# Performance work log

Hardware: AMD Instinct MI355X
Metric: run time of the kernel (lower is better)

## Reference

```python
import jax, jax.numpy as jnp
import numpy as np
from jax import lax

HEADS = 8
C, H, W = 64, 16, 16
D_K = C // HEADS
SCALE = 1.0 / np.sqrt(D_K * H * W).astype(np.float32)


def conv2d(x, w, b):
    # x: [N, C, H, W], w: [O, I, 3, 3], padding=1
    y = lax.conv_general_dilated(x, w, window_strides=(1, 1),
                                 padding=((1, 1), (1, 1)),
                                 dimension_numbers=('NCHW', 'OIHW', 'NCHW'))
    return y + b[None, :, None, None]


def _project(x, w, b, bs, seq):
    # x: [bs, seq, C, H, W] -> conv per frame -> [bs, heads, seq, d_k*H*W]
    y = conv2d(x.reshape(bs * seq, C, H, W), w, b)
    y = y.reshape(bs, seq, HEADS, D_K, H, W)
    y = jnp.transpose(y, (0, 2, 1, 3, 4, 5)).reshape(bs, HEADS, seq, D_K * H * W)
    return y


def setup_inputs() -> dict:
    key = jax.random.key(0)
    ks = jax.random.split(key, 11)
    shp = (2, 256, C, H, W)
    wstd = 1.0 / np.sqrt(C * 9)  # torch Conv2d default init scale
    inp = {
        'q': jax.random.normal(ks[0], shp, jnp.float32),
        'k': jax.random.normal(ks[1], shp, jnp.float32),
        'v': jax.random.normal(ks[2], shp, jnp.float32),
        'Wq': jax.random.uniform(ks[3], (C, C, 3, 3), jnp.float32, -wstd, wstd),
        'bq': jax.random.uniform(ks[4], (C,), jnp.float32, -wstd, wstd),
        'Wk': jax.random.uniform(ks[5], (C, C, 3, 3), jnp.float32, -wstd, wstd),
        'bk': jax.random.uniform(ks[6], (C,), jnp.float32, -wstd, wstd),
        'Wv': jax.random.uniform(ks[7], (C, C, 3, 3), jnp.float32, -wstd, wstd),
        'bv': jax.random.uniform(ks[8], (C,), jnp.float32, -wstd, wstd),
        'Wo': jax.random.uniform(ks[9], (C, C, 3, 3), jnp.float32, -wstd, wstd),
        'bo': jax.random.uniform(ks[10], (C,), jnp.float32, -wstd, wstd),
    }
    return inp


def reference(q, k, v, Wq, bq, Wk, bk, Wv, bv, Wo, bo):
    bs, seq = q.shape[0], q.shape[1]
    qh = _project(q, Wq, bq, bs, seq)  # [bs, h, seq, d_k*H*W]
    kh = _project(k, Wk, bk, bs, seq)
    vh = _project(v, Wv, bv, bs, seq)
    scores = jnp.einsum('bhqd,bhkd->bhqk', qh, kh) * SCALE
    attn = jax.nn.softmax(scores, axis=-1)
    out = jnp.einsum('bhqk,bhkd->bhqd', attn, vh)  # [bs, h, seq, d_k*H*W]
    out = out.reshape(bs, HEADS, seq, D_K, H, W)
    concat = jnp.transpose(out, (0, 2, 1, 3, 4, 5)).reshape(bs * seq, C, H, W)
    y = conv2d(concat, Wo, bo).reshape(bs, seq, C, H, W)
    return y
```

## Files before the change

kernel.cpp:

```cpp
#include <hip/hip_runtime.h>
#include <hip/hip_bf16.h>
#include <hip/hip_fp16.h>

typedef unsigned short u16;
typedef _Float16 f16x8 __attribute__((ext_vector_type(8)));
typedef u16 u16x8 __attribute__((ext_vector_type(8)));
typedef u16 u16x4 __attribute__((ext_vector_type(4)));
typedef float f32x4 __attribute__((ext_vector_type(4)));

__device__ __forceinline__ u16 f2h(float f){
  __half h = __float2half(f);
  return *(u16*)&h;
}

__device__ __forceinline__ void cp16_async(const u16* g, u16* l){
  __builtin_amdgcn_global_load_lds(
      (const __attribute__((address_space(1))) unsigned int*)g,
      (__attribute__((address_space(3))) unsigned int*)l,
      16, 0, 0);
}

__device__ __forceinline__ void prep_w_body(const float* W, u16* Wt, int i){
  if (i >= 36864) return;
  int co = i / 576, rem = i % 576, ci = rem / 9, tap = rem % 9;
  int n = co >> 4, lr = co & 15, kk = ci >> 5, lg = (ci >> 3) & 3, j = ci & 7;
  int s = tap*2 + kk;
  Wt[(((s*4 + n)*64) + lg*16 + lr)*8 + j] = f2h(W[i]);
}

__global__ __launch_bounds__(256) void prep_w3(
    const float* __restrict__ Wq, const float* __restrict__ Wk,
    const float* __restrict__ Wv, u16* __restrict__ Wt)
{
  int which = blockIdx.y;
  const float* W = (which == 0) ? Wq : (which == 1) ? Wk : Wv;
  prep_w_body(W, Wt + which*36864, blockIdx.x * 256 + threadIdx.x);
}

__global__ __launch_bounds__(256) void prep_w(
    const float* __restrict__ W, u16* __restrict__ Wt)
{
  prep_w_body(W, Wt, blockIdx.x * 256 + threadIdx.x);
}

template<bool IN_F32, bool OUT_PROJ>
__device__ __forceinline__ void conv_body(
    const void* __restrict__ xin, const u16* __restrict__ Wt,
    const float* __restrict__ bias, void* __restrict__ dst,
    int frame, u16* xT, int tid)
{
  const int p = tid, py = p >> 4, px = p & 15;
  const int pp = (py + 1)*18 + px + 1;
  const float* xf = (const float*)xin + (size_t)frame * 16384;
  const u16*   xb = (const u16*)  xin + (size_t)frame * 16384;

  float xvf[64];
  u16   xvu[64];
  if (IN_F32){
    #pragma unroll
    for (int c = 0; c < 64; ++c) xvf[c] = xf[c*256 + p];
  } else {
    #pragma unroll
    for (int c = 0; c < 64; ++c) xvu[c] = xb[c*256 + p];
  }

  for (int i = tid; i < 2592; i += 256)
    *(uint4*)((char*)xT + i*16) = make_uint4(0u, 0u, 0u, 0u);
  __syncthreads();

  #pragma unroll
  for (int cb = 0; cb < 8; ++cb){
    u16x8 pk;
    #pragma unroll
    for (int j = 0; j < 8; ++j)
      pk[j] = IN_F32 ? f2h(xvf[cb*8 + j]) : xvu[cb*8 + j];
    unsigned off = (unsigned)(pp*128) + ((((unsigned)cb + (unsigned)pp) & 7u) << 4);
    *(u16x8*)((char*)xT + off) = pk;
  }
  __syncthreads();

  const int w = tid >> 6, lane = tid & 63, lr = lane & 15, lg = lane >> 4;
  const int pyb = w * 4;

  f32x4 acc[4][4];
  #pragma unroll
  for (int n = 0; n < 4; ++n){
    float b = bias[n*16 + lr];
    #pragma unroll
    for (int m = 0; m < 4; ++m){
      acc[m][n][0] = b; acc[m][n][1] = b; acc[m][n][2] = b; acc[m][n][3] = b;
    }
  }

  #define LOADB(s, B) do {                                                  \
    _Pragma("unroll")                                                       \
    for (int n_ = 0; n_ < 4; ++n_)                                          \
      B[n_] = *(const f16x8*)(Wt + ((((s)*4 + n_)*64) + lane)*8);           \
  } while(0)

  #define STEP(s, B) do {                                                   \
    int tap_ = (s) >> 1, kk_ = (s) & 1;                                     \
    int dy_ = tap_ / 3, dx_ = tap_ - dy_*3;                                 \
    f16x8 af_[4];                                                           \
    _Pragma("unroll")                                                       \
    for (int m_ = 0; m_ < 4; ++m_){                                         \
      int pp_ = (pyb + m_ + dy_)*18 + lr + dx_;                             \
      unsigned slot_ = ((unsigned)(kk_*4 + lg) + (unsigned)pp_) & 7u;       \
      af_[m_] = *(const f16x8*)((const char*)xT                             \
                 + (unsigned)(pp_*128) + (slot_ << 4));                     \
    }                                                                       \
    _Pragma("unroll")                                                       \
    for (int m_ = 0; m_ < 4; ++m_)                                          \
      _Pragma("unroll")                                                     \
      for (int n_ = 0; n_ < 4; ++n_)                                        \
        acc[m_][n_] = __builtin_amdgcn_mfma_f32_16x16x32_f16(               \
            af_[m_], B[n_], acc[m_][n_], 0, 0, 0);                          \
  } while(0)

  f16x8 Ba[4], Bb[4];
  LOADB(0, Ba);
  #pragma unroll 1
  for (int it = 0; it < 9; ++it){
    LOADB(it*2 + 1, Bb);
    STEP(it*2, Ba);
    if (it < 8) LOADB(it*2 + 2, Ba);
    STEP(it*2 + 1, Bb);
  }
  #undef LOADB
  #undef STEP

  __syncthreads();
  char* xTc = (char*)xT;
  if (OUT_PROJ){
    #pragma unroll
    for (int n = 0; n < 4; ++n){
      int co = n*16 + lr;
      #pragma unroll
      for (int m = 0; m < 4; ++m){
        int px0 = w*64 + m*16 + lg*4;
        int s = px0 >> 3;
        unsigned aw = (unsigned)(co*512) + (unsigned)((s ^ (co & 7)) << 4)
                      + (unsigned)((px0 & 7) * 2);
        u16x4 o4;
        #pragma unroll
        for (int r = 0; r < 4; ++r) o4[r] = f2h(acc[m][n][r]);
        *(u16x4*)(xTc + aw) = o4;
      }
    }
    __syncthreads();
    u16* d = (u16*)dst;
    const int b = frame >> 8, sq = frame & 255;
    #pragma unroll
    for (int i = 0; i < 8; ++i){
      int c = w*8 + i;
      int co = c*2 + (lane >> 5);
      int pxo = (lane & 31) * 8;
      unsigned ld = (unsigned)(co*512) + (unsigned)(((lane & 31) ^ (co & 7)) << 4);
      uint4 v = *(const uint4*)(xTc + ld);
      int h = co >> 3, dk = co & 7;
      u16* gp = d + ((size_t)((b*8 + h)*256 + sq))*2048 + dk*256 + pxo;
      *(uint4*)gp = v;
    }
  } else {
    float* dfr = (float*)dst + (size_t)frame * 16384;
    #pragma unroll
    for (int ph2 = 0; ph2 < 2; ++ph2){
      if ((w >> 1) == ph2){
        #pragma unroll
        for (int n = 0; n < 4; ++n){
          int co = n*16 + lr;
          #pragma unroll
          for (int m = 0; m < 4; ++m){
            int pxl = (w & 1)*64 + m*16 + lg*4;
            int s = pxl >> 2;
            unsigned aw = (unsigned)(co*512) + (unsigned)((s ^ (co & 7)) << 4);
            *(f32x4*)(xTc + aw) = acc[m][n];
          }
        }
      }
      __syncthreads();
      #pragma unroll
      for (int i = 0; i < 8; ++i){
        int c = w*8 + i;
        int co = c*2 + (lane >> 5);
        int pxl = (lane & 31) * 4;
        unsigned ld = (unsigned)(co*512) + (unsigned)(((lane & 31) ^ (co & 7)) << 4);
        f32x4 v = *(const f32x4*)(xTc + ld);
        *(f32x4*)(dfr + co*256 + ph2*128 + pxl) = v;
      }
      if (ph2 == 0) __syncthreads();
    }
  }
}

__global__ __launch_bounds__(256, 3) void conv3_mfma(
    const float* __restrict__ q, const float* __restrict__ k,
    const float* __restrict__ v, const u16* __restrict__ Wt3,
    const float* __restrict__ bq, const float* __restrict__ bk,
    const float* __restrict__ bv,
    u16* __restrict__ qh, u16* __restrict__ kh, u16* __restrict__ vh)
{
  __shared__ __align__(16) u16 xT[324 * 64];
  const int which = blockIdx.x >> 9;
  const int frame = blockIdx.x & 511;
  const float* x = (which == 0) ? q : (which == 1) ? k : v;
  const float* bias = (which == 0) ? bq : (which == 1) ? bk : bv;
  u16* dst = (which == 0) ? qh : (which == 1) ? kh : vh;
  conv_body<true, true>(x, Wt3 + which*36864, bias, dst, frame, xT, threadIdx.x);
}

__global__ __launch_bounds__(256, 3) void conv_out_mfma(
    const u16* __restrict__ xin, const u16* __restrict__ Wt,
    const float* __restrict__ bias, float* __restrict__ out)
{
  __shared__ __align__(16) u16 xT[324 * 64];
  conv_body<false, false>(xin, Wt, bias, out, blockIdx.x, xT, threadIdx.x);
}

__global__ __launch_bounds__(256) void transpose_v(
    const u16* __restrict__ vh, u16* __restrict__ vt)
{
  __shared__ u16 tile[64][72];
  const int tid = threadIdx.x;
  const int dt = blockIdx.x, st = blockIdx.y, bh = blockIdx.z;
  {
    int r = tid >> 2, c4 = tid & 3;
    const u16* src = vh + ((size_t)(bh*256 + st*64 + r))*2048 + dt*64 + c4*16;
    uint4 v0 = *(const uint4*)src;
    uint4 v1 = *(const uint4*)(src + 8);
    *(uint4*)&tile[r][c4*16]     = v0;
    *(uint4*)&tile[r][c4*16 + 8] = v1;
  }
  __syncthreads();
  {
    int dr = tid >> 2, s4 = tid & 3;
    u16 tmp[16];
    #pragma unroll
    for (int i = 0; i < 16; ++i) tmp[i] = tile[s4*16 + i][dr];
    u16* dstp = vt + ((size_t)(bh*2048 + dt*64 + dr))*256 + st*64 + s4*16;
    *(uint4*)dstp       = *(uint4*)&tmp[0];
    *(uint4*)(dstp + 8) = *(uint4*)&tmp[8];
  }
}

__global__ __launch_bounds__(512, 2) void attn_kernel(
    const u16* __restrict__ qh, const u16* __restrict__ kh,
    const u16* __restrict__ vt, u16* __restrict__ obuf)
{
  const float SCALE = 0.022097086912079608f;
  __shared__ __align__(16) u16 Qs[16*2048];
  __shared__ __align__(16) u16 Kb[2][16384];
  __shared__ __align__(16) u16 P[16*256];
  __shared__ float redA[8][16];
  __shared__ float redB[8][16];

  const int tid = threadIdx.x;
  const int w = tid >> 6, lane = tid & 63, lr = lane & 15, lg = lane >> 4;

  const int id = blockIdx.x;
  const int xcd = id & 7, j = id >> 3;
  const int bh = xcd + 8*(j & 1), qt = j >> 1;
  const int q0 = qt * 16, b = bh >> 3, h = bh & 7;

  const u16* Qg = qh + ((size_t)(bh*256 + q0))*2048;
  const u16* Kg = kh + (size_t)bh * 256 * 2048;
  const u16* Vg = vt + (size_t)bh * 2048 * 256;

  const int spK = (lane & 7) ^ ((lane >> 3) & 7);
  #define STAGE_K(c, buf)                                                   \
    _Pragma("unroll")                                                       \
    for (int r_ = 0; r_ < 4; ++r_)                                          \
      cp16_async(Kg + (size_t)(w*32 + r_*8 + (lane>>3))*2048 + (c)*64 + spK*8, \
                 (buf) + w*2048 + r_*512);

  #define STAGE_V(c, buf)                                                   \
    _Pragma("unroll")                                                       \
    for (int r_ = 0; r_ < 8; ++r_){                                         \
      int rl_ = w*16 + r_*2 + (lane>>5);                                    \
      int sp_ = (lane & 31) ^ (rl_ & 7);                                    \
      cp16_async(Vg + (size_t)((c)*128 + rl_)*256 + sp_*8,                  \
                 (buf) + w*4096 + r_*512);                                  \
    }

  #pragma unroll
  for (int r = 0; r < 8; ++r){
    int t = r*64 + lane;
    int row = w*2 + (t >> 8);
    int dp = t & 255;
    int sp = (dp & ~7) | ((dp & 7) ^ (row & 7));
    cp16_async(Qg + (size_t)row*2048 + sp*8, Qs + w*4096 + r*512);
  }
  STAGE_K(0, Kb[0]);
  __syncthreads();

  const f32x4 zero4 = {0.f, 0.f, 0.f, 0.f};
  f32x4 sacc[2] = {zero4, zero4};
  #pragma unroll 1
  for (int c = 0; c < 32; ++c){
    if (c < 31) STAGE_K(c+1, Kb[(c+1)&1]);
    const u16* kb = Kb[c&1];
    #pragma unroll
    for (int d2 = 0; d2 < 2; ++d2){
      unsigned aoff = (((unsigned)lr << 12) + (unsigned)(c*128 + d2*64 + lg*16))
                      ^ (unsigned)((lr & 7) << 4);
      f16x8 a = *(const f16x8*)((const char*)Qs + aoff);
      #pragma unroll
      for (int n = 0; n < 2; ++n){
        int row = w*32 + n*16 + lr;
        const u16* kp = kb + row*64 + (((d2*4 + lg) ^ (row & 7)) << 3);
        f16x8 bk = *(const f16x8*)kp;
        sacc[n] = __builtin_amdgcn_mfma_f32_16x16x32_f16(a, bk, sacc[n], 0,0,0);
      }
    }
    __syncthreads();
  }

  float mx[4];
  #pragma unroll
  for (int r = 0; r < 4; ++r){
    float vv = fmaxf(sacc[0][r], sacc[1][r]);
    #pragma unroll
    for (int off = 1; off < 16; off <<= 1) vv = fmaxf(vv, __shfl_xor(vv, off));
    mx[r] = vv;
  }
  if (lr == 0){
    #pragma unroll
    for (int r = 0; r < 4; ++r) redA[w][lg*4 + r] = mx[r];
  }
  __syncthreads();
  #pragma unroll
  for (int r = 0; r < 4; ++r){
    int row = lg*4 + r;
    float vv = redA[0][row];
    #pragma unroll
    for (int ww = 1; ww < 8; ++ww) vv = fmaxf(vv, redA[ww][row]);
    mx[r] = vv;
  }

  const int kbase = w * 32;
  float sm[4] = {0.f, 0.f, 0.f, 0.f};
  #pragma unroll
  for (int n = 0; n < 2; ++n)
    #pragma unroll
    for (int r = 0; r < 4; ++r){
      float pv = __expf((sacc[n][r] - mx[r]) * SCALE);
      sm[r] += pv;
      int row = lg*4 + r;
      int col = kbase + n*16 + lr;
      unsigned off = (((unsigned)row << 9) + ((unsigned)col << 1))
                     ^ (unsigned)((row & 7) << 4);
      *(u16*)((char*)P + off) = f2h(pv);
    }
  #pragma unroll
  for (int r = 0; r < 4; ++r){
    float vv = sm[r];
    #pragma unroll
    for (int off = 1; off < 16; off <<= 1) vv += __shfl_xor(vv, off);
    sm[r] = vv;
  }
  if (lr == 0){
    #pragma unroll
    for (int r = 0; r < 4; ++r) redB[w][lg*4 + r] = sm[r];
  }
  __syncthreads();
  float rs[4];
  #pragma unroll
  for (int r = 0; r < 4; ++r){
    int row = lg*4 + r;
    float s = redB[0][row];
    #pragma unroll
    for (int ww = 1; ww < 8; ++ww) s += redB[ww][row];
    rs[r] = 1.0f / s;
  }

  u16* Vb0 = Qs;
  u16* Vb1 = &Kb[0][0];
  STAGE_V(0, Vb0);
  __syncthreads();
  #pragma unroll 1
  for (int c = 0; c < 16; ++c){
    if (c < 15){
      u16* nbuf = ((c+1) & 1) ? Vb1 : Vb0;
      STAGE_V(c+1, nbuf);
    }
    const u16* vb = (c & 1) ? Vb1 : Vb0;
    f32x4 oacc = zero4;
    #pragma unroll
    for (int kt = 0; kt < 8; ++kt){
      unsigned poff = (((unsigned)lr << 9) + (unsigned)(kt*64 + lg*16))
                      ^ (unsigned)((lr & 7) << 4);
      f16x8 pa = *(const f16x8*)((const char*)P + poff);
      int row = w*16 + lr;
      const u16* vp = vb + row*256 + (((kt*4 + lg) ^ (row & 7)) << 3);
      f16x8 bv = *(const f16x8*)vp;
      oacc = __builtin_amdgcn_mfma_f32_16x16x32_f16(pa, bv, oacc, 0,0,0);
    }
    #pragma unroll
    for (int r = 0; r < 4; ++r){
      float o = oacc[r] * rs[r];
      int qrow = q0 + lg*4 + r;
      int d = c*128 + w*16 + lr;
      int frame = b*256 + qrow;
      int cdim = h*8 + (d >> 8);
      obuf[((size_t)(frame*64 + cdim))*256 + (d & 255)] = f2h(o);
    }
    __syncthreads();
  }
  #undef STAGE_K
  #undef STAGE_V
}

extern "C" void kernel_launch(void* const* d_in, const int* in_sizes, int n_in,
                              void* d_out, int out_size, void* d_ws, size_t ws_size,
                              hipStream_t stream)
{
  const float* q  = (const float*)d_in[0];
  const float* k  = (const float*)d_in[1];
  const float* v  = (const float*)d_in[2];
  const float* Wq = (const float*)d_in[3];
  const float* bq = (const float*)d_in[4];
  const float* Wk = (const float*)d_in[5];
  const float* bk = (const float*)d_in[6];
  const float* Wv = (const float*)d_in[7];
  const float* bv = (const float*)d_in[8];
  const float* Wo = (const float*)d_in[9];
  const float* bo = (const float*)d_in[10];
  float* out = (float*)d_out;

  char* ws = (char*)d_ws;
  u16* qh = (u16*)(ws);
  u16* kh = (u16*)(ws + (size_t)16*1024*1024);
  u16* vh = (u16*)(ws + (size_t)32*1024*1024);
  u16* vt = (u16*)(ws + (size_t)48*1024*1024);
  u16* obuf = vh;
  u16* Wt3  = vt;
  u16* WtO  = qh;

  prep_w3<<<dim3(144, 3), dim3(256), 0, stream>>>(Wq, Wk, Wv, Wt3);
  conv3_mfma<<<dim3(1536), dim3(256), 0, stream>>>(q, k, v, Wt3, bq, bk, bv,
                                                   qh, kh, vh);
  transpose_v<<<dim3(32, 4, 16), dim3(256), 0, stream>>>(vh, vt);
  attn_kernel<<<dim3(256), dim3(512), 0, stream>>>(qh, kh, vt, obuf);
  prep_w<<<dim3(144), dim3(256), 0, stream>>>(Wo, WtO);
  conv_out_mfma<<<dim3(512), dim3(256), 0, stream>>>(obuf, WtO, bo, out);
}
```

Before: 115.4 us.

## Store attention output pre-swizzled and DMA it directly into conv LDS tile

The attention kernel now writes its fp16 output in the padded, swizzled LDS layout that the output convolution expects. The output conv then loads each frame with async global-to-LDS copies (global_load_lds) and only zeroes the halo rows, instead of loading 64 scalar channels per thread, zeroing the whole tile and repacking. This removes register staging and an extra LDS pass in conv_out. The cost is scattered 2-byte stores from the attention epilogue and a layout coupling between the two kernels.

```diff
diff --git a/kernel.cpp b/kernel.cpp
--- a/kernel.cpp
+++ b/kernel.cpp
@@ -43,43 +43,57 @@
   prep_w_body(W, Wt, blockIdx.x * 256 + threadIdx.x);
 }
 
-template<bool IN_F32, bool OUT_PROJ>
+template<bool IN_F32, bool OUT_PROJ, bool IN_DMA>
 __device__ __forceinline__ void conv_body(
     const void* __restrict__ xin, const u16* __restrict__ Wt,
     const float* __restrict__ bias, void* __restrict__ dst,
     int frame, u16* xT, int tid)
 {
-  const int p = tid, py = p >> 4, px = p & 15;
-  const int pp = (py + 1)*18 + px + 1;
-  const float* xf = (const float*)xin + (size_t)frame * 16384;
-  const u16*   xb = (const u16*)  xin + (size_t)frame * 16384;
-
-  float xvf[64];
-  u16   xvu[64];
-  if (IN_F32){
+  const int w = tid >> 6, lane = tid & 63, lr = lane & 15, lg = lane >> 4;
+
+  if (IN_DMA){
+    const u16* src = (const u16*)xin + (size_t)frame * 16384;
+    #pragma unroll
+    for (int i2 = 0; i2 < 8; ++i2){
+      int y = w*4 + (i2 >> 1), half = i2 & 1;
+      int basepp = (y + 1)*18 + 1 + half*8;
+      cp16_async(src + (size_t)y*1024 + half*512 + lane*8,
+                 xT + basepp*64 + lane*8);
+    }
+    for (int i = tid; i < 544; i += 256){
+      int r = i >> 3, q = i & 7;
+      int row;
+      if (r < 19)      row = r;
+      else if (r < 49){ int pr = r - 19; row = 18*(1 + (pr >> 1)) + 17 + (pr & 1); }
+      else             row = 305 + (r - 49);
+      *(uint4*)((char*)xT + row*128 + q*16) = make_uint4(0u,0u,0u,0u);
+    }
+    __syncthreads();
+  } else {
+    const int p = tid, py = p >> 4, px = p & 15;
+    const int pp = (py + 1)*18 + px + 1;
+    const float* xf = (const float*)xin + (size_t)frame * 16384;
+
+    float xvf[64];
     #pragma unroll
     for (int c = 0; c < 64; ++c) xvf[c] = xf[c*256 + p];
-  } else {
-    #pragma unroll
-    for (int c = 0; c < 64; ++c) xvu[c] = xb[c*256 + p];
-  }
-
-  for (int i = tid; i < 2592; i += 256)
-    *(uint4*)((char*)xT + i*16) = make_uint4(0u, 0u, 0u, 0u);
-  __syncthreads();
-
-  #pragma unroll
-  for (int cb = 0; cb < 8; ++cb){
-    u16x8 pk;
-    #pragma unroll
-    for (int j = 0; j < 8; ++j)
-      pk[j] = IN_F32 ? f2h(xvf[cb*8 + j]) : xvu[cb*8 + j];
-    unsigned off = (unsigned)(pp*128) + ((((unsigned)cb + (unsigned)pp) & 7u) << 4);
-    *(u16x8*)((char*)xT + off) = pk;
-  }
-  __syncthreads();
-
-  const int w = tid >> 6, lane = tid & 63, lr = lane & 15, lg = lane >> 4;
+
+    for (int i = tid; i < 2592; i += 256)
+      *(uint4*)((char*)xT + i*16) = make_uint4(0u, 0u, 0u, 0u);
+    __builtin_amdgcn_sched_barrier(0);
+    __syncthreads();
+
+    #pragma unroll
+    for (int cb = 0; cb < 8; ++cb){
+      u16x8 pk;
+      #pragma unroll
+      for (int j = 0; j < 8; ++j) pk[j] = f2h(xvf[cb*8 + j]);
+      unsigned off = (unsigned)(pp*128) + ((((unsigned)cb + (unsigned)pp) & 7u) << 4);
+      *(u16x8*)((char*)xT + off) = pk;
+    }
+    __syncthreads();
+  }
+
   const int pyb = w * 4;
 
   f32x4 acc[4][4];
@@ -206,7 +220,7 @@
   const float* x = (which == 0) ? q : (which == 1) ? k : v;
   const float* bias = (which == 0) ? bq : (which == 1) ? bk : bv;
   u16* dst = (which == 0) ? qh : (which == 1) ? kh : vh;
-  conv_body<true, true>(x, Wt3 + which*36864, bias, dst, frame, xT, threadIdx.x);
+  conv_body<true, true, false>(x, Wt3 + which*36864, bias, dst, frame, xT, threadIdx.x);
 }
 
 __global__ __launch_bounds__(256, 3) void conv_out_mfma(
@@ -214,7 +228,7 @@
     const float* __restrict__ bias, float* __restrict__ out)
 {
   __shared__ __align__(16) u16 xT[324 * 64];
-  conv_body<false, false>(xin, Wt, bias, out, blockIdx.x, xT, threadIdx.x);
+  conv_body<false, false, true>(xin, Wt, bias, out, blockIdx.x, xT, threadIdx.x);
 }
 
 __global__ __launch_bounds__(256) void transpose_v(
@@ -401,8 +415,14 @@
       int qrow = q0 + lg*4 + r;
       int d = c*128 + w*16 + lr;
       int frame = b*256 + qrow;
-      int cdim = h*8 + (d >> 8);
-      obuf[((size_t)(frame*64 + cdim))*256 + (d & 255)] = f2h(o);
+      int ci = h*8 + (d >> 8);
+      int p2 = d & 255;
+      int y = p2 >> 4, xcol = p2 & 15;
+      int pp2 = (y + 1)*18 + xcol + 1;
+      int slot = ((ci >> 3) + pp2) & 7;
+      int l2 = ((xcol & 7) << 3) | slot;
+      int half = xcol >> 3;
+      obuf[(size_t)frame*16384 + y*1024 + half*512 + l2*8 + (ci & 7)] = f2h(o);
     }
     __syncthreads();
   }
```

Result: slower. 194.5 us (+68.6%).

## Split QKV projection conv into half-frame blocks with halo for more parallelism

Applied to the files above, without the earlier changes.

The fused Q/K/V projection convolution now processes half a frame (8 output rows plus a 1-row halo) per block instead of a whole frame. This doubles the grid to 3072 blocks, shrinks shared memory and accumulators, and raises the occupancy hint to 6 blocks per CU to improve latency hiding and load balance. In exchange, the halo rows are loaded twice, only 144 of 256 threads do the input staging, and the generic conv body template is replaced by two specialised kernels.

```diff
diff --git a/kernel.cpp b/kernel.cpp
--- a/kernel.cpp
+++ b/kernel.cpp
@@ -43,51 +43,61 @@
   prep_w_body(W, Wt, blockIdx.x * 256 + threadIdx.x);
 }
 
-template<bool IN_F32, bool OUT_PROJ>
-__device__ __forceinline__ void conv_body(
-    const void* __restrict__ xin, const u16* __restrict__ Wt,
-    const float* __restrict__ bias, void* __restrict__ dst,
-    int frame, u16* xT, int tid)
-{
-  const int p = tid, py = p >> 4, px = p & 15;
-  const int pp = (py + 1)*18 + px + 1;
-  const float* xf = (const float*)xin + (size_t)frame * 16384;
-  const u16*   xb = (const u16*)  xin + (size_t)frame * 16384;
+__global__ __launch_bounds__(256, 6) void conv3_half(
+    const float* __restrict__ q, const float* __restrict__ k,
+    const float* __restrict__ v, const u16* __restrict__ Wt3,
+    const float* __restrict__ bq, const float* __restrict__ bk,
+    const float* __restrict__ bv,
+    u16* __restrict__ qh, u16* __restrict__ kh, u16* __restrict__ vh)
+{
+  __shared__ __align__(16) u16 xT[180 * 64];
+  const int tid = threadIdx.x;
+  const int bx = blockIdx.x;
+  const int gf = bx >> 1, half = bx & 1;
+  const int which = gf >> 9, frame = gf & 511;
+  const float* x = (which == 0) ? q : (which == 1) ? k : v;
+  const float* bias = (which == 0) ? bq : (which == 1) ? bk : bv;
+  u16* dout = (which == 0) ? qh : (which == 1) ? kh : vh;
+  const u16* Wt = Wt3 + which*36864;
+  const float* xf = x + (size_t)frame * 16384;
 
   float xvf[64];
-  u16   xvu[64];
-  if (IN_F32){
-    #pragma unroll
-    for (int c = 0; c < 64; ++c) xvf[c] = xf[c*256 + p];
-  } else {
-    #pragma unroll
-    for (int c = 0; c < 64; ++c) xvu[c] = xb[c*256 + p];
-  }
-
-  for (int i = tid; i < 2592; i += 256)
+  int lpp = 0;
+  if (tid < 144){
+    int lyr = tid >> 4, px = tid & 15;
+    int gy = (half == 0) ? lyr : (7 + lyr);
+    int lpy = gy - half*8 + 1;
+    lpp = lpy*18 + px + 1;
+    int p_img = gy*16 + px;
+    #pragma unroll
+    for (int c = 0; c < 64; ++c) xvf[c] = xf[c*256 + p_img];
+  }
+
+  for (int i = tid; i < 1440; i += 256)
     *(uint4*)((char*)xT + i*16) = make_uint4(0u, 0u, 0u, 0u);
   __syncthreads();
 
-  #pragma unroll
-  for (int cb = 0; cb < 8; ++cb){
-    u16x8 pk;
-    #pragma unroll
-    for (int j = 0; j < 8; ++j)
-      pk[j] = IN_F32 ? f2h(xvf[cb*8 + j]) : xvu[cb*8 + j];
-    unsigned off = (unsigned)(pp*128) + ((((unsigned)cb + (unsigned)pp) & 7u) << 4);
-    *(u16x8*)((char*)xT + off) = pk;
+  if (tid < 144){
+    #pragma unroll
+    for (int cb = 0; cb < 8; ++cb){
+      u16x8 pk;
+      #pragma unroll
+      for (int j = 0; j < 8; ++j) pk[j] = f2h(xvf[cb*8 + j]);
+      unsigned off = (unsigned)(lpp*128) + ((((unsigned)cb + (unsigned)lpp) & 7u) << 4);
+      *(u16x8*)((char*)xT + off) = pk;
+    }
   }
   __syncthreads();
 
   const int w = tid >> 6, lane = tid & 63, lr = lane & 15, lg = lane >> 4;
-  const int pyb = w * 4;
-
-  f32x4 acc[4][4];
+  const int pyb = w * 2;
+
+  f32x4 acc[2][4];
   #pragma unroll
   for (int n = 0; n < 4; ++n){
     float b = bias[n*16 + lr];
     #pragma unroll
-    for (int m = 0; m < 4; ++m){
+    for (int m = 0; m < 2; ++m){
       acc[m][n][0] = b; acc[m][n][1] = b; acc[m][n][2] = b; acc[m][n][3] = b;
     }
   }
@@ -101,16 +111,16 @@
   #define STEP(s, B) do {                                                   \
     int tap_ = (s) >> 1, kk_ = (s) & 1;                                     \
     int dy_ = tap_ / 3, dx_ = tap_ - dy_*3;                                 \
-    f16x8 af_[4];                                                           \
-    _Pragma("unroll")                                                       \
-    for (int m_ = 0; m_ < 4; ++m_){                                         \
+    f16x8 af_[2];                                                           \
+    _Pragma("unroll")                                                       \
+    for (int m_ = 0; m_ < 2; ++m_){                                         \
       int pp_ = (pyb + m_ + dy_)*18 + lr + dx_;                             \
       unsigned slot_ = ((unsigned)(kk_*4 + lg) + (unsigned)pp_) & 7u;       \
       af_[m_] = *(const f16x8*)((const char*)xT                             \
                  + (unsigned)(pp_*128) + (slot_ << 4));                     \
     }                                                                       \
     _Pragma("unroll")                                                       \
-    for (int m_ = 0; m_ < 4; ++m_)                                          \
+    for (int m_ = 0; m_ < 2; ++m_)                                          \
       _Pragma("unroll")                                                     \
       for (int n_ = 0; n_ < 4; ++n_)                                        \
         acc[m_][n_] = __builtin_amdgcn_mfma_f32_16x16x32_f16(               \
@@ -131,90 +141,148 @@
 
   __syncthreads();
   char* xTc = (char*)xT;
-  if (OUT_PROJ){
-    #pragma unroll
-    for (int n = 0; n < 4; ++n){
-      int co = n*16 + lr;
+  #pragma unroll
+  for (int n = 0; n < 4; ++n){
+    int co = n*16 + lr;
+    #pragma unroll
+    for (int m = 0; m < 2; ++m){
+      int px0 = w*32 + m*16 + lg*4;
+      int s = px0 >> 3;
+      unsigned aw = (unsigned)(co*256) + (unsigned)((s ^ (co & 7)) << 4)
+                    + (unsigned)((px0 & 7) * 2);
+      u16x4 o4;
       #pragma unroll
-      for (int m = 0; m < 4; ++m){
-        int px0 = w*64 + m*16 + lg*4;
-        int s = px0 >> 3;
-        unsigned aw = (unsigned)(co*512) + (unsigned)((s ^ (co & 7)) << 4)
-                      + (unsigned)((px0 & 7) * 2);
-        u16x4 o4;
+      for (int r = 0; r < 4; ++r) o4[r] = f2h(acc[m][n][r]);
+      *(u16x4*)(xTc + aw) = o4;
+    }
+  }
+  __syncthreads();
+  {
+    const int b = frame >> 8, sq = frame & 255;
+    #pragma unroll
+    for (int i = 0; i < 4; ++i){
+      int c = w*4 + i;
+      int co = c*4 + (lane >> 4);
+      int pxo = (lane & 15) * 8;
+      unsigned ld = (unsigned)(co*256) + (unsigned)(((lane & 15) ^ (co & 7)) << 4);
+      uint4 vv = *(const uint4*)(xTc + ld);
+      int h = co >> 3, dk = co & 7;
+      u16* gp = dout + ((size_t)((b*8 + h)*256 + sq))*2048 + dk*256
+                + half*128 + pxo;
+      *(uint4*)gp = vv;
+    }
+  }
+}
+
+__global__ __launch_bounds__(256, 3) void conv_out_mfma(
+    const u16* __restrict__ xin, const u16* __restrict__ Wt,
+    const float* __restrict__ bias, float* __restrict__ out)
+{
+  __shared__ __align__(16) u16 xT[324 * 64];
+  const int tid = threadIdx.x;
+  const int frame = blockIdx.x;
+  const int p = tid, py = p >> 4, px = p & 15;
+  const int pp = (py + 1)*18 + px + 1;
+  const u16* xb = xin + (size_t)frame * 16384;
+
+  u16 xvu[64];
+  #pragma unroll
+  for (int c = 0; c < 64; ++c) xvu[c] = xb[c*256 + p];
+
+  for (int i = tid; i < 2592; i += 256)
+    *(uint4*)((char*)xT + i*16) = make_uint4(0u, 0u, 0u, 0u);
+  __syncthreads();
+
+  #pragma unroll
+  for (int cb = 0; cb < 8; ++cb){
+    u16x8 pk;
+    #pragma unroll
+    for (int j = 0; j < 8; ++j) pk[j] = xvu[cb*8 + j];
+    unsigned off = (unsigned)(pp*128) + ((((unsigned)cb + (unsigned)pp) & 7u) << 4);
+    *(u16x8*)((char*)xT + off) = pk;
+  }
+  __syncthreads();
+
+  const int w = tid >> 6, lane = tid & 63, lr = lane & 15, lg = lane >> 4;
+  const int pyb = w * 4;
+
+  f32x4 acc[4][4];
+  #pragma unroll
+  for (int n = 0; n < 4; ++n){
+    float b = bias[n*16 + lr];
+    #pragma unroll
+    for (int m = 0; m < 4; ++m){
+      acc[m][n][0] = b; acc[m][n][1] = b; acc[m][n][2] = b; acc[m][n][3] = b;
+    }
+  }
+
+  #define LOADB(s, B) do {                                                  \
+    _Pragma("unroll")                                                       \
+    for (int n_ = 0; n_ < 4; ++n_)                                          \
+      B[n_] = *(const f16x8*)(Wt + ((((s)*4 + n_)*64) + lane)*8);           \
+  } while(0)
+
+  #define STEP(s, B) do {                                                   \
+    int tap_ = (s) >> 1, kk_ = (s) & 1;                                     \
+    int dy_ = tap_ / 3, dx_ = tap_ - dy_*3;                                 \
+    f16x8 af_[4];                                                           \
+    _Pragma("unroll")                                                       \
+    for (int m_ = 0; m_ < 4; ++m_){                                         \
+      int pp_ = (pyb + m_ + dy_)*18 + lr + dx_;                             \
+      unsigned slot_ = ((unsigned)(kk_*4 + lg) + (unsigned)pp_) & 7u;       \
+      af_[m_] = *(const f16x8*)((const char*)xT                             \
+                 + (unsigned)(pp_*128) + (slot_ << 4));                     \
+    }                                                                       \
+    _Pragma("unroll")                                                       \
+    for (int m_ = 0; m_ < 4; ++m_)                                          \
+      _Pragma("unroll")                                                     \
+      for (int n_ = 0; n_ < 4; ++n_)                                        \
+        acc[m_][n_] = __builtin_amdgcn_mfma_f32_16x16x32_f16(               \
+            af_[m_], B[n_], acc[m_][n_], 0, 0, 0);                          \
+  } while(0)
+
+  f16x8 Ba[4], Bb[4];
+  LOADB(0, Ba);
+  #pragma unroll 1
+  for (int it = 0; it < 9; ++it){
+    LOADB(it*2 + 1, Bb);
+    STEP(it*2, Ba);
+    if (it < 8) LOADB(it*2 + 2, Ba);
+    STEP(it*2 + 1, Bb);
+  }
+  #undef LOADB
+  #undef STEP
+
+  __syncthreads();
+  char* xTc = (char*)xT;
+  float* dfr = out + (size_t)frame * 16384;
+  #pragma unroll
+  for (int ph2 = 0; ph2 < 2; ++ph2){
+    if ((w >> 1) == ph2){
+      #pragma unroll
+      for (int n = 0; n < 4; ++n){
+        int co = n*16 + lr;
         #pragma unroll
-        for (int r = 0; r < 4; ++r) o4[r] = f2h(acc[m][n][r]);
-        *(u16x4*)(xTc + aw) = o4;
+        for (int m = 0; m < 4; ++m){
+          int pxl = (w & 1)*64 + m*16 + lg*4;
+          int s = pxl >> 2;
+          unsigned aw = (unsigned)(co*512) + (unsigned)((s ^ (co & 7)) << 4);
+          *(f32x4*)(xTc + aw) = acc[m][n];
+        }
       }
     }
     __syncthreads();
-    u16* d = (u16*)dst;
-    const int b = frame >> 8, sq = frame & 255;
     #pragma unroll
     for (int i = 0; i < 8; ++i){
       int c = w*8 + i;
       int co = c*2 + (lane >> 5);
-      int pxo = (lane & 31) * 8;
+      int pxl = (lane & 31) * 4;
       unsigned ld = (unsigned)(co*512) + (unsigned)(((lane & 31) ^ (co & 7)) << 4);
-      uint4 v = *(const uint4*)(xTc + ld);
-      int h = co >> 3, dk = co & 7;
-      u16* gp = d + ((size_t)((b*8 + h)*256 + sq))*2048 + dk*256 + pxo;
-      *(uint4*)gp = v;
-    }
-  } else {
-    float* dfr = (float*)dst + (size_t)frame * 16384;
-    #pragma unroll
-    for (int ph2 = 0; ph2 < 2; ++ph2){
-      if ((w >> 1) == ph2){
-        #pragma unroll
-        for (int n = 0; n < 4; ++n){
-          int co = n*16 + lr;
-          #pragma unroll
-          for (int m = 0; m < 4; ++m){
-            int pxl = (w & 1)*64 + m*16 + lg*4;
-            int s = pxl >> 2;
-            unsigned aw = (unsigned)(co*512) + (unsigned)((s ^ (co & 7)) << 4);
-            *(f32x4*)(xTc + aw) = acc[m][n];
-          }
-        }
-      }
-      __syncthreads();
-      #pragma unroll
-      for (int i = 0; i < 8; ++i){
-        int c = w*8 + i;
-        int co = c*2 + (lane >> 5);
-        int pxl = (lane & 31) * 4;
-        unsigned ld = (unsigned)(co*512) + (unsigned)(((lane & 31) ^ (co & 7)) << 4);
-        f32x4 v = *(const f32x4*)(xTc + ld);
-        *(f32x4*)(dfr + co*256 + ph2*128 + pxl) = v;
-      }
-      if (ph2 == 0) __syncthreads();
-    }
-  }
-}
-
-__global__ __launch_bounds__(256, 3) void conv3_mfma(
-    const float* __restrict__ q, const float* __restrict__ k,
-    const float* __restrict__ v, const u16* __restrict__ Wt3,
-    const float* __restrict__ bq, const float* __restrict__ bk,
-    const float* __restrict__ bv,
-    u16* __restrict__ qh, u16* __restrict__ kh, u16* __restrict__ vh)
-{
-  __shared__ __align__(16) u16 xT[324 * 64];
-  const int which = blockIdx.x >> 9;
-  const int frame = blockIdx.x & 511;
-  const float* x = (which == 0) ? q : (which == 1) ? k : v;
-  const float* bias = (which == 0) ? bq : (which == 1) ? bk : bv;
-  u16* dst = (which == 0) ? qh : (which == 1) ? kh : vh;
-  conv_body<true, true>(x, Wt3 + which*36864, bias, dst, frame, xT, threadIdx.x);
-}
-
-__global__ __launch_bounds__(256, 3) void conv_out_mfma(
-    const u16* __restrict__ xin, const u16* __restrict__ Wt,
-    const float* __restrict__ bias, float* __restrict__ out)
-{
-  __shared__ __align__(16) u16 xT[324 * 64];
-  conv_body<false, false>(xin, Wt, bias, out, blockIdx.x, xT, threadIdx.x);
+      f32x4 v = *(const f32x4*)(xTc + ld);
+      *(f32x4*)(dfr + co*256 + ph2*128 + pxl) = v;
+    }
+    if (ph2 == 0) __syncthreads();
+  }
 }
 
 __global__ __launch_bounds__(256) void transpose_v(
@@ -437,7 +505,7 @@
   u16* WtO  = qh;
 
   prep_w3<<<dim3(144, 3), dim3(256), 0, stream>>>(Wq, Wk, Wv, Wt3);
-  conv3_mfma<<<dim3(1536), dim3(256), 0, stream>>>(q, k, v, Wt3, bq, bk, bv,
+  conv3_half<<<dim3(3072), dim3(256), 0, stream>>>(q, k, v, Wt3, bq, bk, bv,
                                                    qh, kh, vh);
   transpose_v<<<dim3(32, 4, 16), dim3(256), 0, stream>>>(vh, vt);
   attn_kernel<<<dim3(256), dim3(512), 0, stream>>>(qh, kh, vt, obuf);
```

Result: slower. 127.0 us (+10.1%).
